# Optimization experiments

Hardware: AMD Instinct MI355X
Metric: run time of the kernel (lower is better)

The kernel has to match this reference:

```python
import jax, jax.numpy as jnp
import numpy as np

N_R = 256          # number of relations
N_HOP_MAX = 3      # max hops
N_E = 200_000      # number of entities
N_T = 1_000_000    # number of KB triples
B = 32             # batch size
D_Q = 768          # BERT question embedding dim
D_IN = D_Q + (N_HOP_MAX - 1) * N_R  # input width of dense_inf / dense_att


def setup_inputs() -> dict:
    key = jax.random.key(0)
    ks = jax.random.split(key, 7)
    x = (jax.random.uniform(ks[0], (B, N_E)) < 0.001).astype(jnp.float32)
    h_q = jax.random.normal(ks[1], (B, D_Q), jnp.float32)
    W_inf = jax.random.normal(ks[2], (N_R, D_IN), jnp.float32) * 0.02
    W_att = jax.random.normal(ks[3], (1, D_IN), jnp.float32) * 0.02
    subj_idx = jax.random.randint(ks[4], (N_T,), 0, N_E, jnp.int32)
    rel_idx = jax.random.randint(ks[5], (N_T,), 0, N_R, jnp.int32)
    obj_idx = jax.random.randint(ks[6], (N_T,), 0, N_E, jnp.int32)
    return {"x": x, "h_q": h_q, "W_inf": W_inf, "W_att": W_att,
            "subj_idx": subj_idx, "rel_idx": rel_idx, "obj_idx": obj_idx,
            "n_hop": N_HOP_MAX}


def _one_step(x, r, subj_idx, rel_idx, obj_idx):
    # Equivalent to ((x @ M_subj.T) * (r @ M_rel.T)) @ M_obj with 0/1
    # indicator matrices: gather - elementwise multiply - scatter-add.
    x_t = jnp.take(x, subj_idx, axis=1)   # (B, N_T)
    r_t = jnp.take(r, rel_idx, axis=1)    # (B, N_T)
    prod = x_t * r_t                       # (B, N_T)
    # scatter-add over triples into object entities: (N_T, B) -> (N_E, B)
    return jax.ops.segment_sum(prod.T, obj_idx, num_segments=x.shape[1]).T


def reference(x, h_q, W_inf, W_att, subj_idx, rel_idx, obj_idx, n_hop):
    rs, cs, xs = [], [], []
    for i in range(n_hop):
        if i:
            # most-recent relation first, then older ones (rs[::-1])
            concat = jnp.concatenate([h_q] + rs[::-1], axis=1)
        else:
            concat = h_q
        pad = jnp.zeros((h_q.shape[0], (N_HOP_MAX - 1 - i) * N_R), h_q.dtype)
        concat = jnp.concatenate([concat, pad], axis=1)  # (B, D_IN)
        r = concat @ W_inf.T   # (B, N_R)
        c = concat @ W_att.T   # (B, 1)
        x = _one_step(x, r, subj_idx, rel_idx, obj_idx)  # (B, N_E)
        rs.append(r)
        cs.append(c)
        xs.append(x)
    a = jax.nn.softmax(jnp.concatenate(cs, axis=1), axis=-1)  # (B, n_hop)
    y = jnp.einsum('bh,bhe->be', a, jnp.stack(xs, axis=1))     # (B, N_E)
    return y
```

## Files before the change

### kernel.cpp

```cpp
#include <hip/hip_runtime.h>

#define N_R   256
#define N_E   200000
#define N_T   1000000
#define D_Q   768
#define D_IN  1280

template <bool BN>
__device__ __forceinline__ void hop_quad(
        const float* __restrict__ xIn, const unsigned* __restrict__ maskIn,
        const float* __restrict__ rT,
        const int4* __restrict__ subj4, const int4* __restrict__ rel4,
        const int4* __restrict__ obj4,
        float* __restrict__ xOut, unsigned* __restrict__ maskOut,
        int gb, int t) {
    int tid = gb * 256 + t;
    if (tid >= N_T / 4) return;
    int4 s4 = subj4[tid];
    unsigned m0 = maskIn[s4.x], m1 = maskIn[s4.y];
    unsigned m2 = maskIn[s4.z], m3 = maskIn[s4.w];
    if (!(m0 | m1 | m2 | m3)) return;
    int4 r4 = rel4[tid];
    int4 o4 = obj4[tid];
    int      ss[4] = {s4.x, s4.y, s4.z, s4.w};
    unsigned mk[4] = {m0, m1, m2, m3};
    int      rr[4] = {r4.x, r4.y, r4.z, r4.w};
    int      oo[4] = {o4.x, o4.y, o4.z, o4.w};
#pragma unroll
    for (int k = 0; k < 4; ++k) {
        unsigned mm = mk[k];
        if (!mm) continue;
        int s = ss[k], o = oo[k];
        const float* rrow = rT + rr[k] * 32;
        while (mm) {
            int bb = __ffs(mm) - 1;
            mm &= mm - 1;
            float v = BN ? xIn[(size_t)bb * N_E + s] : xIn[(size_t)s * 32 + bb];
            unsafeAtomicAdd(&xOut[(size_t)o * 32 + bb], v * rrow[bb]);
        }
        atomicOr(&maskOut[o], mk[k]);
    }
}

__global__ void kA(const float* __restrict__ x, const float* __restrict__ h_q,
                   const float* __restrict__ W_inf,
                   unsigned* __restrict__ mask0, unsigned* __restrict__ mask1,
                   unsigned* __restrict__ mask2,
                   float4* __restrict__ outv, float* __restrict__ rT0) {
    __shared__ float hs[32 * 257];
    __shared__ float red[256];
    int t = threadIdx.x;
    if (blockIdx.x < 782) {
        int tid = blockIdx.x * 256 + t;
        float4 z = {0.f, 0.f, 0.f, 0.f};
        for (int i = tid; i < 1600000; i += 782 * 256) outv[i] = z;
        if (tid < N_E) {
            unsigned m = 0;
#pragma unroll 8
            for (int b = 0; b < 32; ++b)
                m |= (x[(size_t)b * N_E + tid] != 0.f ? 1u : 0u) << b;
            mask0[tid] = m;
            mask1[tid] = 0u;
            mask2[tid] = 0u;
        }
    } else {
        int rel = blockIdx.x - 782;
        int b = t & 31, kp = t >> 5;
        float acc = 0.f;
        for (int c = 0; c < 3; ++c) {
            __syncthreads();
#pragma unroll
            for (int i = 0; i < 32; ++i)
                hs[i * 257 + t] = h_q[i * D_Q + c * 256 + t];
            __syncthreads();
            const float* w = &W_inf[rel * D_IN + c * 256 + kp * 32];
#pragma unroll
            for (int i = 0; i < 32; ++i)
                acc += w[i] * hs[b * 257 + kp * 32 + i];
        }
        red[t] = acc;
        __syncthreads();
        if (t < 32) {
            float s = 0.f;
            for (int q = 0; q < 8; ++q) s += red[q * 32 + t];
            rT0[rel * 32 + t] = s;
        }
    }
}

__global__ void kB(const float* __restrict__ W_inf, const float* __restrict__ rT0,
                   float* __restrict__ rT1,
                   const float* __restrict__ x, const unsigned* __restrict__ mask0,
                   const int4* __restrict__ subj4, const int4* __restrict__ rel4,
                   const int4* __restrict__ obj4,
                   float* __restrict__ bufA, unsigned* __restrict__ mask1) {
    __shared__ float red[256];
    int t = threadIdx.x;
    if (blockIdx.x < 256) {
        int relb = blockIdx.x;
        int b = t & 31, jp = t >> 5;
        const float* w2 = &W_inf[relb * D_IN + D_Q];
        float acc = 0.f;
#pragma unroll 8
        for (int jj = 0; jj < 32; ++jj) {
            int j = jp * 32 + jj;
            acc += w2[j] * rT0[j * 32 + b];
        }
        red[t] = acc;
        __syncthreads();
        if (t < 32) {
            float s = rT0[relb * 32 + t];
            for (int q = 0; q < 8; ++q) s += red[q * 32 + t];
            rT1[relb * 32 + t] = s;
        }
    } else {
        hop_quad<true>(x, mask0, rT0, subj4, rel4, obj4, bufA, mask1,
                       blockIdx.x - 256, t);
    }
}

__global__ void kC(const float* __restrict__ W_inf, const float* __restrict__ W_att,
                   const float* __restrict__ h_q,
                   const float* __restrict__ rT0, const float* __restrict__ rT1,
                   float* __restrict__ rT2, float* __restrict__ a_w,
                   const float* __restrict__ bufA, const unsigned* __restrict__ mask1,
                   const int4* __restrict__ subj4, const int4* __restrict__ rel4,
                   const int4* __restrict__ obj4,
                   float* __restrict__ bufB, unsigned* __restrict__ mask2) {
    __shared__ float red[256];
    __shared__ float p0[256], p1[256], p2[256], p3[256];
    int t = threadIdx.x;
    if (blockIdx.x < 256) {
        int relb = blockIdx.x;
        int b = t & 31, jp = t >> 5;
        const float* w2 = &W_inf[relb * D_IN + D_Q];
        const float* w3 = w2 + N_R;
        float acc = 0.f;
#pragma unroll 8
        for (int jj = 0; jj < 32; ++jj) {
            int j = jp * 32 + jj;
            acc += w2[j] * rT1[j * 32 + b] + w3[j] * rT0[j * 32 + b];
        }
        red[t] = acc;
        __syncthreads();
        if (t < 32) {
            float s = rT0[relb * 32 + t];
            for (int q = 0; q < 8; ++q) s += red[q * 32 + t];
            rT2[relb * 32 + t] = s;
        }
    } else if (blockIdx.x == 256) {
        int b = t & 31, p = t >> 5;
        float c0 = 0.f;
        for (int k = p * 96; k < p * 96 + 96; ++k) c0 += W_att[k] * h_q[b * D_Q + k];
        float s1 = 0.f, s2 = 0.f, s3 = 0.f;
        for (int j = p * 32; j < p * 32 + 32; ++j) {
            float w2 = W_att[D_Q + j], w3 = W_att[D_Q + N_R + j];
            float r0v = rT0[j * 32 + b], r1v = rT1[j * 32 + b];
            s1 += w2 * r0v; s2 += w2 * r1v; s3 += w3 * r0v;
        }
        p0[t] = c0; p1[t] = s1; p2[t] = s2; p3[t] = s3;
        __syncthreads();
        if (t < 32) {
            float C0 = 0.f, S1 = 0.f, S2 = 0.f, S3 = 0.f;
            for (int q = 0; q < 8; ++q) {
                C0 += p0[q * 32 + t]; S1 += p1[q * 32 + t];
                S2 += p2[q * 32 + t]; S3 += p3[q * 32 + t];
            }
            float c1 = C0 + S1, c2 = C0 + S2 + S3;
            float m  = fmaxf(C0, fmaxf(c1, c2));
            float e0 = __expf(C0 - m), e1 = __expf(c1 - m), e2 = __expf(c2 - m);
            float inv = 1.f / (e0 + e1 + e2);
            a_w[t] = e0 * inv; a_w[32 + t] = e1 * inv; a_w[64 + t] = e2 * inv;
        }
    } else {
        hop_quad<false>(bufA, mask1, rT1, subj4, rel4, obj4, bufB, mask2,
                        blockIdx.x - 257, t);
    }
}

__global__ void kDE(const float* __restrict__ bufA, const float* __restrict__ bufB,
                    const unsigned* __restrict__ mask1,
                    const unsigned* __restrict__ mask2,
                    const float* __restrict__ rT2, const float* __restrict__ a_w,
                    const int4* __restrict__ subj4, const int4* __restrict__ rel4,
                    const int4* __restrict__ obj4, float* __restrict__ out) {
    __shared__ float a0s[32], a1s[32], a2s[32];
    int t = threadIdx.x;
    if (t < 32) { a0s[t] = a_w[t]; a1s[t] = a_w[32 + t]; a2s[t] = a_w[64 + t]; }
    __syncthreads();
    if (blockIdx.x < 977) {
        int tid = blockIdx.x * 256 + t;
        if (tid >= N_T / 4) return;
        int4 s4 = subj4[tid];
        unsigned m0 = mask2[s4.x], m1 = mask2[s4.y];
        unsigned m2 = mask2[s4.z], m3 = mask2[s4.w];
        if (!(m0 | m1 | m2 | m3)) return;
        int4 r4 = rel4[tid];
        int4 o4 = obj4[tid];
        int      ss[4] = {s4.x, s4.y, s4.z, s4.w};
        unsigned mk[4] = {m0, m1, m2, m3};
        int      rr[4] = {r4.x, r4.y, r4.z, r4.w};
        int      oo[4] = {o4.x, o4.y, o4.z, o4.w};
#pragma unroll
        for (int k = 0; k < 4; ++k) {
            unsigned mm = mk[k];
            if (!mm) continue;
            const float* rrow = rT2 + rr[k] * 32;
            const float* xrow = bufB + (size_t)ss[k] * 32;
            int o = oo[k];
            while (mm) {
                int bb = __ffs(mm) - 1;
                mm &= mm - 1;
                unsafeAtomicAdd(&out[(size_t)bb * N_E + o],
                                a2s[bb] * xrow[bb] * rrow[bb]);
            }
        }
    } else {
        int e = (blockIdx.x - 977) * 256 + t;
        if (e >= N_E) return;
        unsigned m1v = mask1[e], m2v = mask2[e];
        unsigned mu = m1v | m2v;
        if (!mu) return;
        const float* r1 = bufA + (size_t)e * 32;
        const float* r2 = bufB + (size_t)e * 32;
        while (mu) {
            int bb = __ffs(mu) - 1;
            mu &= mu - 1;
            float c = 0.f;
            if ((m1v >> bb) & 1) c += a0s[bb] * r1[bb];
            if ((m2v >> bb) & 1) c += a1s[bb] * r2[bb];
            unsafeAtomicAdd(&out[(size_t)bb * N_E + e], c);
        }
    }
}

extern "C" void kernel_launch(void* const* d_in, const int* in_sizes, int n_in,
                              void* d_out, int out_size, void* d_ws, size_t ws_size,
                              hipStream_t stream) {
    const float* x     = (const float*)d_in[0];
    const float* h_q   = (const float*)d_in[1];
    const float* W_inf = (const float*)d_in[2];
    const float* W_att = (const float*)d_in[3];
    const int*   subj  = (const int*)d_in[4];
    const int*   rel   = (const int*)d_in[5];
    const int*   obj   = (const int*)d_in[6];
    float* out = (float*)d_out;

    const size_t NEB = (size_t)N_E * 32;
    float*    bufA  = (float*)d_ws;
    float*    bufB  = bufA + NEB;
    float*    rT0   = bufB + NEB;
    float*    rT1   = rT0 + N_R * 32;
    float*    rT2   = rT1 + N_R * 32;
    float*    a_w   = rT2 + N_R * 32;
    unsigned* mask0 = (unsigned*)(a_w + 96);
    unsigned* mask1 = mask0 + N_E;
    unsigned* mask2 = mask1 + N_E;

    kA<<<782 + 256, 256, 0, stream>>>(x, h_q, W_inf, mask0, mask1, mask2,
                                      (float4*)out, rT0);
    kB<<<256 + 977, 256, 0, stream>>>(W_inf, rT0, rT1, x, mask0,
                                      (const int4*)subj, (const int4*)rel,
                                      (const int4*)obj, bufA, mask1);
    kC<<<257 + 977, 256, 0, stream>>>(W_inf, W_att, h_q, rT0, rT1, rT2, a_w,
                                      bufA, mask1, (const int4*)subj,
                                      (const int4*)rel, (const int4*)obj,
                                      bufB, mask2);
    kDE<<<977 + 782, 256, 0, stream>>>(bufA, bufB, mask1, mask2, rT2, a_w,
                                       (const int4*)subj, (const int4*)rel,
                                       (const int4*)obj, out);
}
```

Baseline: 195.6 us.

## Move hop-1 output accumulation into kC and halve triples per thread in kDE

The hop-1 contribution (a0 * bufA) to the output is now written by extra blocks in kC, which run alongside the hop-2 scatter. Those blocks recompute the softmax weight a0 locally from W_att, h_q, rT0 and rT1 in a 32-thread serial loop. kDE now handles only the hop-2 and hop-3 terms and processes two triples per thread instead of four, doubling its block count to spread sparse work more evenly. The redundant per-block softmax recomputation adds serial work in each of the 782 new blocks.

```diff
diff --git a/kernel.cpp b/kernel.cpp
--- a/kernel.cpp
+++ b/kernel.cpp
@@ -126,7 +126,8 @@
                    const float* __restrict__ bufA, const unsigned* __restrict__ mask1,
                    const int4* __restrict__ subj4, const int4* __restrict__ rel4,
                    const int4* __restrict__ obj4,
-                   float* __restrict__ bufB, unsigned* __restrict__ mask2) {
+                   float* __restrict__ bufB, unsigned* __restrict__ mask2,
+                   float* __restrict__ out) {
     __shared__ float red[256];
     __shared__ float p0[256], p1[256], p2[256], p3[256];
     int t = threadIdx.x;
@@ -172,37 +173,63 @@
             float inv = 1.f / (e0 + e1 + e2);
             a_w[t] = e0 * inv; a_w[32 + t] = e1 * inv; a_w[64 + t] = e2 * inv;
         }
-    } else {
+    } else if (blockIdx.x < 1234) {
         hop_quad<false>(bufA, mask1, rT1, subj4, rel4, obj4, bufB, mask2,
                         blockIdx.x - 257, t);
-    }
-}
-
-__global__ void kDE(const float* __restrict__ bufA, const float* __restrict__ bufB,
-                    const unsigned* __restrict__ mask1,
+    } else {
+        __shared__ float a0l[32];
+        if (t < 32) {
+            int b = t;
+            float c0 = 0.f;
+            for (int k = 0; k < D_Q; ++k) c0 += W_att[k] * h_q[b * D_Q + k];
+            float s1 = 0.f, s2 = 0.f, s3 = 0.f;
+            for (int j = 0; j < N_R; ++j) {
+                float w2 = W_att[D_Q + j], w3 = W_att[D_Q + N_R + j];
+                float r0v = rT0[j * 32 + b], r1v = rT1[j * 32 + b];
+                s1 += w2 * r0v; s2 += w2 * r1v; s3 += w3 * r0v;
+            }
+            float C0 = c0, c1 = C0 + s1, c2 = C0 + s2 + s3;
+            float m  = fmaxf(C0, fmaxf(c1, c2));
+            float e0 = __expf(C0 - m), e1 = __expf(c1 - m), e2 = __expf(c2 - m);
+            a0l[t] = e0 / (e0 + e1 + e2);
+        }
+        __syncthreads();
+        int e = (blockIdx.x - 1234) * 256 + t;
+        if (e >= N_E) return;
+        unsigned m1v = mask1[e];
+        if (!m1v) return;
+        const float* r1 = bufA + (size_t)e * 32;
+        while (m1v) {
+            int bb = __ffs(m1v) - 1;
+            m1v &= m1v - 1;
+            unsafeAtomicAdd(&out[(size_t)bb * N_E + e], a0l[bb] * r1[bb]);
+        }
+    }
+}
+
+__global__ void kDE(const float* __restrict__ bufB,
                     const unsigned* __restrict__ mask2,
                     const float* __restrict__ rT2, const float* __restrict__ a_w,
-                    const int4* __restrict__ subj4, const int4* __restrict__ rel4,
-                    const int4* __restrict__ obj4, float* __restrict__ out) {
-    __shared__ float a0s[32], a1s[32], a2s[32];
-    int t = threadIdx.x;
-    if (t < 32) { a0s[t] = a_w[t]; a1s[t] = a_w[32 + t]; a2s[t] = a_w[64 + t]; }
+                    const int2* __restrict__ subj2, const int2* __restrict__ rel2,
+                    const int2* __restrict__ obj2, float* __restrict__ out) {
+    __shared__ float a1s[32], a2s[32];
+    int t = threadIdx.x;
+    if (t < 32) { a1s[t] = a_w[32 + t]; a2s[t] = a_w[64 + t]; }
     __syncthreads();
-    if (blockIdx.x < 977) {
+    if (blockIdx.x < 1954) {
         int tid = blockIdx.x * 256 + t;
-        if (tid >= N_T / 4) return;
-        int4 s4 = subj4[tid];
-        unsigned m0 = mask2[s4.x], m1 = mask2[s4.y];
-        unsigned m2 = mask2[s4.z], m3 = mask2[s4.w];
-        if (!(m0 | m1 | m2 | m3)) return;
-        int4 r4 = rel4[tid];
-        int4 o4 = obj4[tid];
-        int      ss[4] = {s4.x, s4.y, s4.z, s4.w};
-        unsigned mk[4] = {m0, m1, m2, m3};
-        int      rr[4] = {r4.x, r4.y, r4.z, r4.w};
-        int      oo[4] = {o4.x, o4.y, o4.z, o4.w};
-#pragma unroll
-        for (int k = 0; k < 4; ++k) {
+        if (tid >= N_T / 2) return;
+        int2 s2 = subj2[tid];
+        unsigned m0 = mask2[s2.x], m1 = mask2[s2.y];
+        if (!(m0 | m1)) return;
+        int2 r2 = rel2[tid];
+        int2 o2 = obj2[tid];
+        int      ss[2] = {s2.x, s2.y};
+        unsigned mk[2] = {m0, m1};
+        int      rr[2] = {r2.x, r2.y};
+        int      oo[2] = {o2.x, o2.y};
+#pragma unroll
+        for (int k = 0; k < 2; ++k) {
             unsigned mm = mk[k];
             if (!mm) continue;
             const float* rrow = rT2 + rr[k] * 32;
@@ -216,20 +243,15 @@
             }
         }
     } else {
-        int e = (blockIdx.x - 977) * 256 + t;
+        int e = (blockIdx.x - 1954) * 256 + t;
         if (e >= N_E) return;
-        unsigned m1v = mask1[e], m2v = mask2[e];
-        unsigned mu = m1v | m2v;
-        if (!mu) return;
-        const float* r1 = bufA + (size_t)e * 32;
+        unsigned m2v = mask2[e];
+        if (!m2v) return;
         const float* r2 = bufB + (size_t)e * 32;
-        while (mu) {
-            int bb = __ffs(mu) - 1;
-            mu &= mu - 1;
-            float c = 0.f;
-            if ((m1v >> bb) & 1) c += a0s[bb] * r1[bb];
-            if ((m2v >> bb) & 1) c += a1s[bb] * r2[bb];
-            unsafeAtomicAdd(&out[(size_t)bb * N_E + e], c);
+        while (m2v) {
+            int bb = __ffs(m2v) - 1;
+            m2v &= m2v - 1;
+            unsafeAtomicAdd(&out[(size_t)bb * N_E + e], a1s[bb] * r2[bb]);
         }
     }
 }
@@ -262,11 +284,11 @@
     kB<<<256 + 977, 256, 0, stream>>>(W_inf, rT0, rT1, x, mask0,
                                       (const int4*)subj, (const int4*)rel,
                                       (const int4*)obj, bufA, mask1);
-    kC<<<257 + 977, 256, 0, stream>>>(W_inf, W_att, h_q, rT0, rT1, rT2, a_w,
-                                      bufA, mask1, (const int4*)subj,
-                                      (const int4*)rel, (const int4*)obj,
-                                      bufB, mask2);
-    kDE<<<977 + 782, 256, 0, stream>>>(bufA, bufB, mask1, mask2, rT2, a_w,
-                                       (const int4*)subj, (const int4*)rel,
-                                       (const int4*)obj, out);
-}
+    kC<<<257 + 977 + 782, 256, 0, stream>>>(W_inf, W_att, h_q, rT0, rT1, rT2,
+                                            a_w, bufA, mask1, (const int4*)subj,
+                                            (const int4*)rel, (const int4*)obj,
+                                            bufB, mask2, out);
+    kDE<<<1954 + 782, 256, 0, stream>>>(bufB, mask2, rT2, a_w,
+                                        (const int2*)subj, (const int2*)rel,
+                                        (const int2*)obj, out);
+}
```

Measured after the change: 203.3 us. 1.04x slower.
